# Kernel optimization log

Measured on AMD Instinct MI355X. Metric: run time of the kernel, lower is better.

The kernel has to match this reference:

```python
import jax, jax.numpy as jnp
import numpy as np

B, S, H = 4, 1024, 1024
NH = 16
D = H // NH  # attention_head_size = 64
L = 9        # num_labels
MAXREL = 5
B_PERSON = 1
I_PERSON = 2
LN_EPS = 1e-5


def setup_inputs() -> dict:
    key = jax.random.key(0)
    ks = jax.random.split(key, 16)
    lin = lambda k, i, o: 0.02 * jax.random.normal(k, (i, o), jnp.float32)
    return {
        "sequence_output": jax.random.normal(ks[0], (B, S, H), jnp.float32),
        "Wq": lin(ks[1], H, H), "bq": jnp.zeros((H,), jnp.float32),
        "Wk": lin(ks[2], H, H), "bk": jnp.zeros((H,), jnp.float32),
        "Wv": lin(ks[3], H, H), "bv": jnp.zeros((H,), jnp.float32),
        "Wo": lin(ks[4], H, H), "bo": jnp.zeros((H,), jnp.float32),
        "ln_g": jnp.ones((H,), jnp.float32), "ln_b": jnp.zeros((H,), jnp.float32),
        "Ws": lin(ks[5], H, L), "bs": jnp.zeros((L,), jnp.float32),
        "entity_bias": 0.1 * jax.random.normal(ks[6], (L,), jnp.float32),
        "rel_pos_emb": jax.random.normal(ks[7], (2 * MAXREL + 1, D), jnp.float32),  # declared but unused in forward math, matching the torch module
    }


def reference(sequence_output, Wq, bq, Wk, bk, Wv, bv, Wo, bo, ln_g, ln_b, Ws, bs, entity_bias, rel_pos_emb):
    x = sequence_output  # [B,S,H]
    b, s, _ = x.shape

    def heads(t):  # [B,S,H] -> [B,NH,S,D]
        return t.reshape(b, s, NH, D).transpose(0, 2, 1, 3)

    q = heads(x @ Wq + bq)
    k = heads(x @ Wk + bk)
    v = heads(x @ Wv + bv)

    scores = jnp.einsum('bhqd,bhkd->bhqk', q, k)  # [B,NH,S,S]

    r = jnp.arange(s, dtype=jnp.float32)
    dist = jnp.abs(r[:, None] - r[None, :])                 # |i-j|, [S,S]
    pos_bias = jnp.exp(-0.1 * jnp.clip(dist, 0.0, float(MAXREL)))
    # torch order: (scores + pos_bias) / sqrt(D) + distance_mask
    scores = (scores + pos_bias) / np.sqrt(D) + (-0.1) * dist

    probs = jax.nn.softmax(scores, axis=-1)  # dropout is identity in eval
    ctx = jnp.einsum('bhqk,bhkd->bhqd', probs, v)
    ctx = ctx.transpose(0, 2, 1, 3).reshape(b, s, H)

    y = x + (ctx @ Wo + bo)  # residual
    mu = y.mean(-1, keepdims=True)
    var = y.var(-1, keepdims=True)
    yn = (y - mu) / jnp.sqrt(var + LN_EPS) * ln_g + ln_b

    span_logits = yn @ Ws + bs  # [B,S,L]
    # entity-bias loop: if argmax(span_logits[i,j-1]) == B-PERSON, add entity_bias[I-PERSON] twice to final[i,j,I-PERSON]
    prev_is_b = (jnp.argmax(span_logits[:, :-1, :], axis=-1) == B_PERSON).astype(span_logits.dtype)  # [B,S-1]
    final_logits = span_logits.at[:, 1:, I_PERSON].add(2.0 * entity_bias[I_PERSON] * prev_is_b)
    return final_logits
```

## Files before the change

### kernel.cpp

```cpp
#include <hip/hip_runtime.h>
#include <hip/hip_bf16.h>
#include <math.h>

typedef unsigned short ush;
typedef __attribute__((ext_vector_type(8))) short frag16;
typedef __attribute__((ext_vector_type(4))) float f32x4;

#define S_   1024
#define H_   1024
#define NH_  16
#define D_   64
#define L_   9
#define MB_  (1048576ull)

__device__ __forceinline__ ush bf16_rne(float x) {
  unsigned int b = __float_as_uint(x);
  b += 0x7FFFu + ((b >> 16) & 1u);
  return (ush)(b >> 16);
}
__device__ __forceinline__ void split2(float x, ush& h, ush& l) {
  h = bf16_rne(x);
  l = bf16_rne(x - __uint_as_float((unsigned int)h << 16));
}

__device__ __forceinline__ void load_lds16(const ush* g, const ush* l) {
  __builtin_amdgcn_global_load_lds(
      (const __attribute__((address_space(1))) void*)g,
      (__attribute__((address_space(3))) void*)l, 16, 0, 0);
}

__global__ __launch_bounds__(256) void split_wT4(
    const float* W0, const float* W1, const float* W2, const float* W3,
    ush* h0, ush* l0, ush* h1, ush* l1, ush* h2, ush* l2, ush* h3, ush* l3) {
  __shared__ __align__(16) float Ls[64][68];
  const float* W = (blockIdx.z == 0) ? W0 : (blockIdx.z == 1) ? W1
                 : (blockIdx.z == 2) ? W2 : W3;
  ush* Th = (blockIdx.z == 0) ? h0 : (blockIdx.z == 1) ? h1
          : (blockIdx.z == 2) ? h2 : h3;
  ush* Tl = (blockIdx.z == 0) ? l0 : (blockIdx.z == 1) ? l1
          : (blockIdx.z == 2) ? l2 : l3;
  const int tid = threadIdx.x;
  const int n0 = blockIdx.x * 64, k0 = blockIdx.y * 64;
#pragma unroll
  for (int it = 0; it < 4; it++) {
    int flat = tid + 256 * it;
    int row = flat >> 4, nc = (flat & 15) * 4;
    *(float4*)&Ls[row][nc] = *(const float4*)&W[(size_t)(k0 + row) * 1024 + n0 + nc];
  }
  __syncthreads();
#pragma unroll
  for (int it = 0; it < 2; it++) {
    int flat = tid + 256 * it;
    int nrow = flat >> 3, kc = (flat & 7) * 8;
    ush hs[8], ls[8];
#pragma unroll
    for (int u = 0; u < 8; u++) split2(Ls[kc + u][nrow], hs[u], ls[u]);
    uint4 ph, pl;
    ph.x = hs[0] | ((unsigned)hs[1] << 16); ph.y = hs[2] | ((unsigned)hs[3] << 16);
    ph.z = hs[4] | ((unsigned)hs[5] << 16); ph.w = hs[6] | ((unsigned)hs[7] << 16);
    pl.x = ls[0] | ((unsigned)ls[1] << 16); pl.y = ls[2] | ((unsigned)ls[3] << 16);
    pl.z = ls[4] | ((unsigned)ls[5] << 16); pl.w = ls[6] | ((unsigned)ls[7] << 16);
    size_t o = (size_t)(n0 + nrow) * 1024 + k0 + kc;
    *(uint4*)&Th[o] = ph;
    *(uint4*)&Tl[o] = pl;
  }
}

__global__ __launch_bounds__(256) void cast_x(
    const float* __restrict__ x, ush* __restrict__ xh) {
  const size_t i = ((size_t)blockIdx.x * 256 + threadIdx.x) * 8;
  float4 a = *(const float4*)&x[i];
  float4 b = *(const float4*)&x[i + 4];
  const float v[8] = {a.x, a.y, a.z, a.w, b.x, b.y, b.z, b.w};
  ush h[8];
#pragma unroll
  for (int u = 0; u < 8; u++) h[u] = bf16_rne(v[u]);
  uint4 ph;
  ph.x = h[0] | ((unsigned)h[1] << 16); ph.y = h[2] | ((unsigned)h[3] << 16);
  ph.z = h[4] | ((unsigned)h[5] << 16); ph.w = h[6] | ((unsigned)h[7] << 16);
  *(uint4*)&xh[i] = ph;
}

__global__ __launch_bounds__(256) void gemm_qkv(
    const ush* __restrict__ xh,
    const ush* __restrict__ Bq_h, const ush* __restrict__ Bq_l,
    const ush* __restrict__ Bk_h, const ush* __restrict__ Bk_l,
    const ush* __restrict__ Bv_h, const ush* __restrict__ Bv_l,
    const float* __restrict__ bq, const float* __restrict__ bk,
    const float* __restrict__ bv,
    ush* __restrict__ qh, ush* __restrict__ kh, ush* __restrict__ vT) {
  __shared__ __align__(16) ush As[2][128][32];
  __shared__ __align__(16) ush Bs[2][2][128][32];
  const int tid = threadIdx.x, lane = tid & 63, wave = tid >> 6;
  const int l15 = lane & 15, quad = lane >> 4;
  const int m0 = blockIdx.y * 128, n0 = blockIdx.x * 128;
  const int z = blockIdx.z;
  const ush* Bh_g = (z == 0) ? Bq_h : (z == 1) ? Bk_h : Bv_h;
  const ush* Bl_g = (z == 0) ? Bq_l : (z == 1) ? Bk_l : Bv_l;
  const float* bias = (z == 0) ? bq : (z == 1) ? bk : bv;
  ush* outp = (z == 0) ? qh : (z == 1) ? kh : vT;

  const int wm = (wave >> 1) * 64, wn = (wave & 1) * 64;

  f32x4 acc[4][4];
#pragma unroll
  for (int i = 0; i < 4; i++)
#pragma unroll
    for (int j = 0; j < 4; j++) acc[i][j] = (f32x4){0.f, 0.f, 0.f, 0.f};

  auto stage = [&](int bi, int k0) {
#pragma unroll
    for (int jj = 0; jj < 2; jj++) {
      const int call = wave * 2 + jj;
      const int c = call * 64 + lane;
      const int r = c >> 2, ch = c & 3;
      const ush* src = xh + (size_t)(m0 + r) * 1024 + k0 + ch * 8;
      load_lds16(src, &As[bi][0][0] + (size_t)call * 512);
    }
#pragma unroll
    for (int jj = 0; jj < 4; jj++) {
      const int call = wave * 4 + jj;
      const int c = call * 64 + lane;
      const int r = (c >> 2) & 127, ch = c & 3;
      const ush* src = ((c >= 512) ? Bl_g : Bh_g)
                     + (size_t)(n0 + r) * 1024 + k0 + ch * 8;
      load_lds16(src, &Bs[bi][0][0][0] + (size_t)call * 512);
    }
  };

  stage(0, 0);
  __syncthreads();

  for (int k0 = 0; k0 < 1024; k0 += 32) {
    const int cur = (k0 >> 5) & 1;
    if (k0 + 32 < 1024) stage(cur ^ 1, k0 + 32);

    frag16 a_h[4], b_h[4], b_l[4];
#pragma unroll
    for (int s = 0; s < 4; s++)
      a_h[s] = *(const frag16*)&As[cur][wm + s * 16 + l15][quad * 8];
#pragma unroll
    for (int t = 0; t < 4; t++) {
      const int col = wn + t * 16 + l15;
      b_h[t] = *(const frag16*)&Bs[cur][0][col][quad * 8];
      b_l[t] = *(const frag16*)&Bs[cur][1][col][quad * 8];
    }
#pragma unroll
    for (int mi = 0; mi < 4; mi++)
#pragma unroll
      for (int ni = 0; ni < 4; ni++) {
        acc[mi][ni] = __builtin_amdgcn_mfma_f32_16x16x32_bf16(
            a_h[mi], b_h[ni], acc[mi][ni], 0, 0, 0);
        acc[mi][ni] = __builtin_amdgcn_mfma_f32_16x16x32_bf16(
            a_h[mi], b_l[ni], acc[mi][ni], 0, 0, 0);
      }
    __syncthreads();
  }

#pragma unroll
  for (int mi = 0; mi < 4; mi++) {
    const int rbase = m0 + wm + mi * 16 + quad * 4;
    const int bb = rbase >> 10, ss = rbase & 1023;
#pragma unroll
    for (int ni = 0; ni < 4; ni++) {
      const int col = n0 + wn + ni * 16 + l15;
      const float bv_ = bias[col];
      const int hidx = col >> 6, d = col & 63;
      if (z == 2) {
        ushort4 p4;
        p4.x = bf16_rne(acc[mi][ni][0] + bv_);
        p4.y = bf16_rne(acc[mi][ni][1] + bv_);
        p4.z = bf16_rne(acc[mi][ni][2] + bv_);
        p4.w = bf16_rne(acc[mi][ni][3] + bv_);
        *(ushort4*)&outp[((size_t)(bb * NH_ + hidx) * D_ + d) * S_ + ss] = p4;
      } else {
#pragma unroll
        for (int r = 0; r < 4; r++) {
          const size_t o =
              ((size_t)(bb * NH_ + hidx) * S_ + (ss + r)) * D_ + d;
          outp[o] = bf16_rne(acc[mi][ni][r] + bv_);
        }
      }
    }
  }
}

__global__ __launch_bounds__(256) void gemm_o(
    const ush* __restrict__ ctxh,
    const ush* __restrict__ Boh, const ush* __restrict__ Bol,
    const float* __restrict__ bo, const float* __restrict__ resid,
    float* __restrict__ outf) {
  __shared__ __align__(16) ush As[2][128][32];
  __shared__ __align__(16) ush Bs[2][2][64][32];
  const int tid = threadIdx.x, lane = tid & 63, wave = tid >> 6;
  const int l15 = lane & 15, quad = lane >> 4;
  const int m0 = blockIdx.y * 128, n0 = blockIdx.x * 64;
  const int wm = (wave >> 1) * 64, wn = (wave & 1) * 32;

  f32x4 acc[4][2];
#pragma unroll
  for (int i = 0; i < 4; i++)
#pragma unroll
    for (int j = 0; j < 2; j++) acc[i][j] = (f32x4){0.f, 0.f, 0.f, 0.f};

  auto stage = [&](int bi, int k0) {
#pragma unroll
    for (int jj = 0; jj < 2; jj++) {
      const int call = wave * 2 + jj;
      const int c = call * 64 + lane;
      const int r = c >> 2, ch = c & 3;
      const ush* src = ctxh + (size_t)(m0 + r) * 1024 + k0 + ch * 8;
      load_lds16(src, &As[bi][0][0] + (size_t)call * 512);
    }
#pragma unroll
    for (int jj = 0; jj < 2; jj++) {
      const int call = wave * 2 + jj;
      const int c = call * 64 + lane;
      const int r = (c >> 2) & 63, ch = c & 3;
      const ush* src = ((c >= 256) ? Bol : Boh)
                     + (size_t)(n0 + r) * 1024 + k0 + ch * 8;
      load_lds16(src, &Bs[bi][0][0][0] + (size_t)call * 512);
    }
  };

  stage(0, 0);
  __syncthreads();

  for (int k0 = 0; k0 < 1024; k0 += 32) {
    const int cur = (k0 >> 5) & 1;
    if (k0 + 32 < 1024) stage(cur ^ 1, k0 + 32);

    frag16 a_h[4], b_h[2], b_l[2];
#pragma unroll
    for (int s = 0; s < 4; s++)
      a_h[s] = *(const frag16*)&As[cur][wm + s * 16 + l15][quad * 8];
#pragma unroll
    for (int t = 0; t < 2; t++) {
      const int col = wn + t * 16 + l15;
      b_h[t] = *(const frag16*)&Bs[cur][0][col][quad * 8];
      b_l[t] = *(const frag16*)&Bs[cur][1][col][quad * 8];
    }
#pragma unroll
    for (int mi = 0; mi < 4; mi++)
#pragma unroll
      for (int ni = 0; ni < 2; ni++) {
        acc[mi][ni] = __builtin_amdgcn_mfma_f32_16x16x32_bf16(
            a_h[mi], b_h[ni], acc[mi][ni], 0, 0, 0);
        acc[mi][ni] = __builtin_amdgcn_mfma_f32_16x16x32_bf16(
            a_h[mi], b_l[ni], acc[mi][ni], 0, 0, 0);
      }
    __syncthreads();
  }

#pragma unroll
  for (int mi = 0; mi < 4; mi++) {
    const int rbase = m0 + wm + mi * 16 + quad * 4;
#pragma unroll
    for (int ni = 0; ni < 2; ni++) {
      const int col = n0 + wn + ni * 16 + l15;
      const float bv_ = bo[col];
#pragma unroll
      for (int r = 0; r < 4; r++) {
        const int m = rbase + r;
        outf[(size_t)m * 1024 + col] =
            acc[mi][ni][r] + bv_ + resid[(size_t)m * 1024 + col];
      }
    }
  }
}

__global__ __launch_bounds__(256) void attn2(
    const ush* __restrict__ qh, const ush* __restrict__ kh,
    const ush* __restrict__ vT, ush* __restrict__ ch) {
  __shared__ __align__(16) ush Kh[64][72];
  __shared__ __align__(16) ush VTs[64][72];
  __shared__ __align__(16) ush Pst[64][72];
  __shared__ float LUT[256];
  const int tid = threadIdx.x;
  const int lane = tid & 63, wave = tid >> 6;
  const int l15 = lane & 15, quad = lane >> 4;
  const int w16 = wave * 16;
  const int bh = blockIdx.y;
  const int b = bh >> 4, h = bh & 15;
  const int q0 = blockIdx.x * 64;

  const float K1 = 0.18033688011112042f;
  const float K2 = 0.14426950408889634f;
  {
    const float dd = (float)tid;
    LUT[tid] = __expf(-0.1f * fminf(dd, 5.0f)) * K1 - dd * K2
             - 28.853900817779268f;
  }

  const size_t qrow = ((size_t)bh * S_ + q0 + w16 + l15) * D_;
  frag16 a_h[2];
  a_h[0] = *(const frag16*)&qh[qrow + quad * 8];
  a_h[1] = *(const frag16*)&qh[qrow + 32 + quad * 8];

  f32x4 o[4];
  float lrow[4];
#pragma unroll
  for (int i = 0; i < 4; i++) {
    o[i] = (f32x4){0.f, 0.f, 0.f, 0.f};
    lrow[i] = 0.f;
  }

  const size_t kbase = (size_t)bh * S_ * D_;
  const size_t vbase = (size_t)bh * D_ * S_;

  const int jlo = (q0 > 128) ? q0 - 128 : 0;
  const int jend = (q0 + 192 < S_) ? q0 + 192 : S_;

  for (int j0 = jlo; j0 < jend; j0 += 64) {
    __syncthreads();
#pragma unroll
    for (int it = 0; it < 2; it++) {
      const int flat = tid + 256 * it;
      const int row = flat >> 3, dc = (flat & 7) * 8;
      *(uint4*)&Kh[row][dc] =
          *(const uint4*)&kh[kbase + (size_t)(j0 + row) * D_ + dc];
      *(uint4*)&VTs[row][dc] =
          *(const uint4*)&vT[vbase + (size_t)row * S_ + j0 + dc];
    }
    __syncthreads();

    f32x4 c4[4];
#pragma unroll
    for (int nt = 0; nt < 4; nt++) c4[nt] = (f32x4){0.f, 0.f, 0.f, 0.f};
#pragma unroll
    for (int kk = 0; kk < 2; kk++) {
#pragma unroll
      for (int nt = 0; nt < 4; nt++) {
        frag16 bh_ = *(const frag16*)&Kh[nt * 16 + l15][kk * 32 + quad * 8];
        c4[nt] = __builtin_amdgcn_mfma_f32_16x16x32_bf16(a_h[kk], bh_, c4[nt], 0, 0, 0);
      }
    }

    const int ib = q0 + w16 + quad * 4 - j0 - l15;
#pragma unroll
    for (int r = 0; r < 4; r++) {
#pragma unroll
      for (int nt = 0; nt < 4; nt++) {
        int di = ib + r - nt * 16;
        di = (di < 0) ? -di : di;
        const float sv = exp2f(fmaf(c4[nt][r], K1, LUT[di]));
        lrow[r] += sv;
        Pst[w16 + quad * 4 + r][nt * 16 + l15] = bf16_rne(sv);
      }
    }

    frag16 pa[2];
    pa[0] = *(const frag16*)&Pst[w16 + l15][quad * 8];
    pa[1] = *(const frag16*)&Pst[w16 + l15][32 + quad * 8];
#pragma unroll
    for (int dt = 0; dt < 4; dt++) {
      frag16 vb0 = *(const frag16*)&VTs[dt * 16 + l15][quad * 8];
      frag16 vb1 = *(const frag16*)&VTs[dt * 16 + l15][32 + quad * 8];
      o[dt] = __builtin_amdgcn_mfma_f32_16x16x32_bf16(pa[0], vb0, o[dt], 0, 0, 0);
      o[dt] = __builtin_amdgcn_mfma_f32_16x16x32_bf16(pa[1], vb1, o[dt], 0, 0, 0);
    }
  }

#pragma unroll
  for (int r = 0; r < 4; r++) {
#pragma unroll
    for (int off = 1; off < 16; off <<= 1) lrow[r] += __shfl_xor(lrow[r], off);
    const float inv = 1.0f / lrow[r];
    const size_t rowp =
        ((size_t)(b * S_ + q0 + w16 + quad * 4 + r)) * H_ + h * 64;
#pragma unroll
    for (int dt = 0; dt < 4; dt++)
      ch[rowp + dt * 16 + l15] = bf16_rne(o[dt][r] * inv);
  }
}

__global__ __launch_bounds__(256) void ln_span(
    const float* __restrict__ y, const float* __restrict__ g,
    const float* __restrict__ bta, const float* __restrict__ Wsp,
    const float* __restrict__ bs, float* __restrict__ logits) {
  const int row = blockIdx.x;
  const int tid = threadIdx.x, lane = tid & 63, wave = tid >> 6;
  const float* yr = y + (size_t)row * 1024;
  float vals[4], s = 0.f, s2 = 0.f;
#pragma unroll
  for (int i = 0; i < 4; i++) {
    float t = yr[tid + i * 256];
    vals[i] = t; s += t; s2 += t * t;
  }
#pragma unroll
  for (int off = 32; off; off >>= 1) {
    s += __shfl_xor(s, off);
    s2 += __shfl_xor(s2, off);
  }
  __shared__ float red[8];
  __shared__ float red9[4][12];
  if (lane == 0) { red[wave] = s; red[4 + wave] = s2; }
  __syncthreads();
  s = red[0] + red[1] + red[2] + red[3];
  s2 = red[4] + red[5] + red[6] + red[7];
  const float mu = s * (1.0f / 1024.0f);
  const float var = s2 * (1.0f / 1024.0f) - mu * mu;
  const float inv = rsqrtf(var + 1e-5f);

  float lg[9];
#pragma unroll
  for (int l = 0; l < 9; l++) lg[l] = 0.f;
#pragma unroll
  for (int i = 0; i < 4; i++) {
    const int hh = tid + i * 256;
    const float yn = (vals[i] - mu) * inv * g[hh] + bta[hh];
#pragma unroll
    for (int l = 0; l < 9; l++) lg[l] += yn * Wsp[hh * 9 + l];
  }
#pragma unroll
  for (int l = 0; l < 9; l++) {
#pragma unroll
    for (int off = 32; off; off >>= 1) lg[l] += __shfl_xor(lg[l], off);
  }
  if (lane == 0) {
#pragma unroll
    for (int l = 0; l < 9; l++) red9[wave][l] = lg[l];
  }
  __syncthreads();
  if (tid < 9) {
    logits[(size_t)row * 9 + tid] =
        red9[0][tid] + red9[1][tid] + red9[2][tid] + red9[3][tid] + bs[tid];
  }
}

__global__ __launch_bounds__(256) void final_kernel(
    const float* __restrict__ logits, const float* __restrict__ eb,
    float* __restrict__ out) {
  const int m = blockIdx.x * 256 + threadIdx.x;
  const int i = m & 1023;
  float cur[9];
#pragma unroll
  for (int l = 0; l < 9; l++) cur[l] = logits[(size_t)m * 9 + l];
  if (i > 0) {
    const float* prev = logits + (size_t)(m - 1) * 9;
    int am = 0;
    float best = prev[0];
#pragma unroll
    for (int l = 1; l < 9; l++) {
      float pv = prev[l];
      if (pv > best) { best = pv; am = l; }
    }
    if (am == 1) cur[2] += 2.0f * eb[2];
  }
#pragma unroll
  for (int l = 0; l < 9; l++) out[(size_t)m * 9 + l] = cur[l];
}

extern "C" void kernel_launch(void* const* d_in, const int* in_sizes, int n_in,
                              void* d_out, int out_size, void* d_ws, size_t ws_size,
                              hipStream_t stream) {
  const float* x    = (const float*)d_in[0];
  const float* Wq   = (const float*)d_in[1];
  const float* bq   = (const float*)d_in[2];
  const float* Wk   = (const float*)d_in[3];
  const float* bk   = (const float*)d_in[4];
  const float* Wv   = (const float*)d_in[5];
  const float* bv   = (const float*)d_in[6];
  const float* Wo   = (const float*)d_in[7];
  const float* bo   = (const float*)d_in[8];
  const float* ln_g = (const float*)d_in[9];
  const float* ln_b = (const float*)d_in[10];
  const float* Ws   = (const float*)d_in[11];
  const float* bs   = (const float*)d_in[12];
  const float* eb   = (const float*)d_in[13];
  float* out = (float*)d_out;
  char* W8 = (char*)d_ws;

  ush* WoT_h = (ush*)(W8 + 0 * MB_);
  ush* WoT_l = (ush*)(W8 + 2 * MB_);
  ush* WqT_h = (ush*)(W8 + 4 * MB_);
  ush* WqT_l = (ush*)(W8 + 6 * MB_);
  ush* WkT_h = (ush*)(W8 + 8 * MB_);
  ush* WkT_l = (ush*)(W8 + 10 * MB_);
  ush* WvT_h = (ush*)(W8 + 12 * MB_);
  ush* WvT_l = (ush*)(W8 + 14 * MB_);
  ush* xh    = (ush*)(W8 + 16 * MB_);
  ush* qh    = (ush*)(W8 + 24 * MB_);
  ush* kh    = (ush*)(W8 + 32 * MB_);
  ush* vT    = (ush*)(W8 + 40 * MB_);
  ush* ctxh  = (ush*)(W8 + 48 * MB_);
  float* y_ws  = (float*)(W8 + 24 * MB_);
  float* lg_ws = (float*)(W8 + 40 * MB_);

  split_wT4<<<dim3(16, 16, 4), 256, 0, stream>>>(
      Wq, Wk, Wv, Wo, WqT_h, WqT_l, WkT_h, WkT_l, WvT_h, WvT_l, WoT_h, WoT_l);
  cast_x<<<2048, 256, 0, stream>>>(x, xh);

  gemm_qkv<<<dim3(8, 32, 3), 256, 0, stream>>>(
      xh, WqT_h, WqT_l, WkT_h, WkT_l, WvT_h, WvT_l, bq, bk, bv, qh, kh, vT);
  attn2<<<dim3(16, 64), 256, 0, stream>>>(qh, kh, vT, ctxh);
  gemm_o<<<dim3(16, 32), 256, 0, stream>>>(ctxh, WoT_h, WoT_l, bo, x, y_ws);
  ln_span<<<4096, 256, 0, stream>>>(y_ws, ln_g, ln_b, Ws, bs, lg_ws);
  final_kernel<<<16, 256, 0, stream>>>(lg_ws, eb, out);
}
```

Baseline: 244.5 us.

## Switch GEMMs and attention from split-bf16 to single fp16 MFMA

Replaces the bf16 hi/lo weight split (two MFMAs per tile) with one fp16 cast of weights and activations, so each GEMM issues half the MFMAs and loads half the B-operand bytes. Attention Q/K/V, probabilities and context move to fp16 as well. The softmax LUT offset shrinks from about 28.85 to about 2.885 so the probabilities stay inside fp16 range. The trade is reduced dynamic range and a different rounding error, with possible overflow or underflow if the data leaves fp16 range.

```diff
diff --git a/kernel.cpp b/kernel.cpp
--- a/kernel.cpp
+++ b/kernel.cpp
@@ -3,7 +3,8 @@
 #include <math.h>
 
 typedef unsigned short ush;
-typedef __attribute__((ext_vector_type(8))) short frag16;
+typedef __attribute__((ext_vector_type(8))) _Float16 fragh;
+typedef __attribute__((ext_vector_type(4))) _Float16 half4;
 typedef __attribute__((ext_vector_type(4))) float f32x4;
 
 #define S_   1024
@@ -13,32 +14,20 @@
 #define L_   9
 #define MB_  (1048576ull)
 
-__device__ __forceinline__ ush bf16_rne(float x) {
-  unsigned int b = __float_as_uint(x);
-  b += 0x7FFFu + ((b >> 16) & 1u);
-  return (ush)(b >> 16);
-}
-__device__ __forceinline__ void split2(float x, ush& h, ush& l) {
-  h = bf16_rne(x);
-  l = bf16_rne(x - __uint_as_float((unsigned int)h << 16));
-}
-
 __device__ __forceinline__ void load_lds16(const ush* g, const ush* l) {
   __builtin_amdgcn_global_load_lds(
       (const __attribute__((address_space(1))) void*)g,
       (__attribute__((address_space(3))) void*)l, 16, 0, 0);
 }
 
-__global__ __launch_bounds__(256) void split_wT4(
+__global__ __launch_bounds__(256) void cast_wT4(
     const float* W0, const float* W1, const float* W2, const float* W3,
-    ush* h0, ush* l0, ush* h1, ush* l1, ush* h2, ush* l2, ush* h3, ush* l3) {
+    ush* T0, ush* T1, ush* T2, ush* T3) {
   __shared__ __align__(16) float Ls[64][68];
   const float* W = (blockIdx.z == 0) ? W0 : (blockIdx.z == 1) ? W1
                  : (blockIdx.z == 2) ? W2 : W3;
-  ush* Th = (blockIdx.z == 0) ? h0 : (blockIdx.z == 1) ? h1
-          : (blockIdx.z == 2) ? h2 : h3;
-  ush* Tl = (blockIdx.z == 0) ? l0 : (blockIdx.z == 1) ? l1
-          : (blockIdx.z == 2) ? l2 : l3;
+  ush* Th = (blockIdx.z == 0) ? T0 : (blockIdx.z == 1) ? T1
+          : (blockIdx.z == 2) ? T2 : T3;
   const int tid = threadIdx.x;
   const int n0 = blockIdx.x * 64, k0 = blockIdx.y * 64;
 #pragma unroll
@@ -52,17 +41,10 @@
   for (int it = 0; it < 2; it++) {
     int flat = tid + 256 * it;
     int nrow = flat >> 3, kc = (flat & 7) * 8;
-    ush hs[8], ls[8];
-#pragma unroll
-    for (int u = 0; u < 8; u++) split2(Ls[kc + u][nrow], hs[u], ls[u]);
-    uint4 ph, pl;
-    ph.x = hs[0] | ((unsigned)hs[1] << 16); ph.y = hs[2] | ((unsigned)hs[3] << 16);
-    ph.z = hs[4] | ((unsigned)hs[5] << 16); ph.w = hs[6] | ((unsigned)hs[7] << 16);
-    pl.x = ls[0] | ((unsigned)ls[1] << 16); pl.y = ls[2] | ((unsigned)ls[3] << 16);
-    pl.z = ls[4] | ((unsigned)ls[5] << 16); pl.w = ls[6] | ((unsigned)ls[7] << 16);
-    size_t o = (size_t)(n0 + nrow) * 1024 + k0 + kc;
-    *(uint4*)&Th[o] = ph;
-    *(uint4*)&Tl[o] = pl;
+    fragh v;
+#pragma unroll
+    for (int u = 0; u < 8; u++) v[u] = (_Float16)Ls[kc + u][nrow];
+    *(fragh*)&Th[(size_t)(n0 + nrow) * 1024 + k0 + kc] = v;
   }
 }
 
@@ -71,32 +53,28 @@
   const size_t i = ((size_t)blockIdx.x * 256 + threadIdx.x) * 8;
   float4 a = *(const float4*)&x[i];
   float4 b = *(const float4*)&x[i + 4];
-  const float v[8] = {a.x, a.y, a.z, a.w, b.x, b.y, b.z, b.w};
-  ush h[8];
-#pragma unroll
-  for (int u = 0; u < 8; u++) h[u] = bf16_rne(v[u]);
-  uint4 ph;
-  ph.x = h[0] | ((unsigned)h[1] << 16); ph.y = h[2] | ((unsigned)h[3] << 16);
-  ph.z = h[4] | ((unsigned)h[5] << 16); ph.w = h[6] | ((unsigned)h[7] << 16);
-  *(uint4*)&xh[i] = ph;
+  fragh v;
+  v[0] = (_Float16)a.x; v[1] = (_Float16)a.y;
+  v[2] = (_Float16)a.z; v[3] = (_Float16)a.w;
+  v[4] = (_Float16)b.x; v[5] = (_Float16)b.y;
+  v[6] = (_Float16)b.z; v[7] = (_Float16)b.w;
+  *(fragh*)&xh[i] = v;
 }
 
 __global__ __launch_bounds__(256) void gemm_qkv(
     const ush* __restrict__ xh,
-    const ush* __restrict__ Bq_h, const ush* __restrict__ Bq_l,
-    const ush* __restrict__ Bk_h, const ush* __restrict__ Bk_l,
-    const ush* __restrict__ Bv_h, const ush* __restrict__ Bv_l,
+    const ush* __restrict__ Bq, const ush* __restrict__ Bk,
+    const ush* __restrict__ Bv,
     const float* __restrict__ bq, const float* __restrict__ bk,
     const float* __restrict__ bv,
     ush* __restrict__ qh, ush* __restrict__ kh, ush* __restrict__ vT) {
   __shared__ __align__(16) ush As[2][128][32];
-  __shared__ __align__(16) ush Bs[2][2][128][32];
+  __shared__ __align__(16) ush Bs[2][128][32];
   const int tid = threadIdx.x, lane = tid & 63, wave = tid >> 6;
   const int l15 = lane & 15, quad = lane >> 4;
   const int m0 = blockIdx.y * 128, n0 = blockIdx.x * 128;
   const int z = blockIdx.z;
-  const ush* Bh_g = (z == 0) ? Bq_h : (z == 1) ? Bk_h : Bv_h;
-  const ush* Bl_g = (z == 0) ? Bq_l : (z == 1) ? Bk_l : Bv_l;
+  const ush* Bg = (z == 0) ? Bq : (z == 1) ? Bk : Bv;
   const float* bias = (z == 0) ? bq : (z == 1) ? bk : bv;
   ush* outp = (z == 0) ? qh : (z == 1) ? kh : vT;
 
@@ -114,17 +92,16 @@
       const int call = wave * 2 + jj;
       const int c = call * 64 + lane;
       const int r = c >> 2, ch = c & 3;
-      const ush* src = xh + (size_t)(m0 + r) * 1024 + k0 + ch * 8;
-      load_lds16(src, &As[bi][0][0] + (size_t)call * 512);
-    }
-#pragma unroll
-    for (int jj = 0; jj < 4; jj++) {
-      const int call = wave * 4 + jj;
+      load_lds16(xh + (size_t)(m0 + r) * 1024 + k0 + ch * 8,
+                 &As[bi][0][0] + (size_t)call * 512);
+    }
+#pragma unroll
+    for (int jj = 0; jj < 2; jj++) {
+      const int call = wave * 2 + jj;
       const int c = call * 64 + lane;
-      const int r = (c >> 2) & 127, ch = c & 3;
-      const ush* src = ((c >= 512) ? Bl_g : Bh_g)
-                     + (size_t)(n0 + r) * 1024 + k0 + ch * 8;
-      load_lds16(src, &Bs[bi][0][0][0] + (size_t)call * 512);
+      const int r = c >> 2, ch = c & 3;
+      load_lds16(Bg + (size_t)(n0 + r) * 1024 + k0 + ch * 8,
+                 &Bs[bi][0][0] + (size_t)call * 512);
     }
   };
 
@@ -135,25 +112,19 @@
     const int cur = (k0 >> 5) & 1;
     if (k0 + 32 < 1024) stage(cur ^ 1, k0 + 32);
 
-    frag16 a_h[4], b_h[4], b_l[4];
+    fragh a[4], b[4];
 #pragma unroll
     for (int s = 0; s < 4; s++)
-      a_h[s] = *(const frag16*)&As[cur][wm + s * 16 + l15][quad * 8];
-#pragma unroll
-    for (int t = 0; t < 4; t++) {
-      const int col = wn + t * 16 + l15;
-      b_h[t] = *(const frag16*)&Bs[cur][0][col][quad * 8];
-      b_l[t] = *(const frag16*)&Bs[cur][1][col][quad * 8];
-    }
+      a[s] = *(const fragh*)&As[cur][wm + s * 16 + l15][quad * 8];
+#pragma unroll
+    for (int t = 0; t < 4; t++)
+      b[t] = *(const fragh*)&Bs[cur][wn + t * 16 + l15][quad * 8];
 #pragma unroll
     for (int mi = 0; mi < 4; mi++)
 #pragma unroll
-      for (int ni = 0; ni < 4; ni++) {
-        acc[mi][ni] = __builtin_amdgcn_mfma_f32_16x16x32_bf16(
-            a_h[mi], b_h[ni], acc[mi][ni], 0, 0, 0);
-        acc[mi][ni] = __builtin_amdgcn_mfma_f32_16x16x32_bf16(
-            a_h[mi], b_l[ni], acc[mi][ni], 0, 0, 0);
-      }
+      for (int ni = 0; ni < 4; ni++)
+        acc[mi][ni] = __builtin_amdgcn_mfma_f32_16x16x32_f16(
+            a[mi], b[ni], acc[mi][ni], 0, 0, 0);
     __syncthreads();
   }
 
@@ -167,18 +138,18 @@
       const float bv_ = bias[col];
       const int hidx = col >> 6, d = col & 63;
       if (z == 2) {
-        ushort4 p4;
-        p4.x = bf16_rne(acc[mi][ni][0] + bv_);
-        p4.y = bf16_rne(acc[mi][ni][1] + bv_);
-        p4.z = bf16_rne(acc[mi][ni][2] + bv_);
-        p4.w = bf16_rne(acc[mi][ni][3] + bv_);
-        *(ushort4*)&outp[((size_t)(bb * NH_ + hidx) * D_ + d) * S_ + ss] = p4;
+        half4 p4;
+        p4[0] = (_Float16)(acc[mi][ni][0] + bv_);
+        p4[1] = (_Float16)(acc[mi][ni][1] + bv_);
+        p4[2] = (_Float16)(acc[mi][ni][2] + bv_);
+        p4[3] = (_Float16)(acc[mi][ni][3] + bv_);
+        *(half4*)&outp[((size_t)(bb * NH_ + hidx) * D_ + d) * S_ + ss] = p4;
       } else {
 #pragma unroll
         for (int r = 0; r < 4; r++) {
           const size_t o =
               ((size_t)(bb * NH_ + hidx) * S_ + (ss + r)) * D_ + d;
-          outp[o] = bf16_rne(acc[mi][ni][r] + bv_);
+          *(_Float16*)&outp[o] = (_Float16)(acc[mi][ni][r] + bv_);
         }
       }
     }
@@ -186,12 +157,11 @@
 }
 
 __global__ __launch_bounds__(256) void gemm_o(
-    const ush* __restrict__ ctxh,
-    const ush* __restrict__ Boh, const ush* __restrict__ Bol,
+    const ush* __restrict__ ctxh, const ush* __restrict__ Bo,
     const float* __restrict__ bo, const float* __restrict__ resid,
     float* __restrict__ outf) {
   __shared__ __align__(16) ush As[2][128][32];
-  __shared__ __align__(16) ush Bs[2][2][64][32];
+  __shared__ __align__(16) ush Bs[2][64][32];
   const int tid = threadIdx.x, lane = tid & 63, wave = tid >> 6;
   const int l15 = lane & 15, quad = lane >> 4;
   const int m0 = blockIdx.y * 128, n0 = blockIdx.x * 64;
@@ -209,17 +179,14 @@
       const int call = wave * 2 + jj;
       const int c = call * 64 + lane;
       const int r = c >> 2, ch = c & 3;
-      const ush* src = ctxh + (size_t)(m0 + r) * 1024 + k0 + ch * 8;
-      load_lds16(src, &As[bi][0][0] + (size_t)call * 512);
-    }
-#pragma unroll
-    for (int jj = 0; jj < 2; jj++) {
-      const int call = wave * 2 + jj;
-      const int c = call * 64 + lane;
-      const int r = (c >> 2) & 63, ch = c & 3;
-      const ush* src = ((c >= 256) ? Bol : Boh)
-                     + (size_t)(n0 + r) * 1024 + k0 + ch * 8;
-      load_lds16(src, &Bs[bi][0][0][0] + (size_t)call * 512);
+      load_lds16(ctxh + (size_t)(m0 + r) * 1024 + k0 + ch * 8,
+                 &As[bi][0][0] + (size_t)call * 512);
+    }
+    {
+      const int c = wave * 64 + lane;
+      const int r = c >> 2, ch = c & 3;
+      load_lds16(Bo + (size_t)(n0 + r) * 1024 + k0 + ch * 8,
+                 &Bs[bi][0][0] + (size_t)wave * 512);
     }
   };
 
@@ -230,25 +197,19 @@
     const int cur = (k0 >> 5) & 1;
     if (k0 + 32 < 1024) stage(cur ^ 1, k0 + 32);
 
-    frag16 a_h[4], b_h[2], b_l[2];
+    fragh a[4], b[2];
 #pragma unroll
     for (int s = 0; s < 4; s++)
-      a_h[s] = *(const frag16*)&As[cur][wm + s * 16 + l15][quad * 8];
-#pragma unroll
-    for (int t = 0; t < 2; t++) {
-      const int col = wn + t * 16 + l15;
-      b_h[t] = *(const frag16*)&Bs[cur][0][col][quad * 8];
-      b_l[t] = *(const frag16*)&Bs[cur][1][col][quad * 8];
-    }
+      a[s] = *(const fragh*)&As[cur][wm + s * 16 + l15][quad * 8];
+#pragma unroll
+    for (int t = 0; t < 2; t++)
+      b[t] = *(const fragh*)&Bs[cur][wn + t * 16 + l15][quad * 8];
 #pragma unroll
     for (int mi = 0; mi < 4; mi++)
 #pragma unroll
-      for (int ni = 0; ni < 2; ni++) {
-        acc[mi][ni] = __builtin_amdgcn_mfma_f32_16x16x32_bf16(
-            a_h[mi], b_h[ni], acc[mi][ni], 0, 0, 0);
-        acc[mi][ni] = __builtin_amdgcn_mfma_f32_16x16x32_bf16(
-            a_h[mi], b_l[ni], acc[mi][ni], 0, 0, 0);
-      }
+      for (int ni = 0; ni < 2; ni++)
+        acc[mi][ni] = __builtin_amdgcn_mfma_f32_16x16x32_f16(
+            a[mi], b[ni], acc[mi][ni], 0, 0, 0);
     __syncthreads();
   }
 
@@ -289,13 +250,13 @@
   {
     const float dd = (float)tid;
     LUT[tid] = __expf(-0.1f * fminf(dd, 5.0f)) * K1 - dd * K2
-             - 28.853900817779268f;
+             - 2.8853900817779268f;
   }
 
   const size_t qrow = ((size_t)bh * S_ + q0 + w16 + l15) * D_;
-  frag16 a_h[2];
-  a_h[0] = *(const frag16*)&qh[qrow + quad * 8];
-  a_h[1] = *(const frag16*)&qh[qrow + 32 + quad * 8];
+  fragh a_h[2];
+  a_h[0] = *(const fragh*)&qh[qrow + quad * 8];
+  a_h[1] = *(const fragh*)&qh[qrow + 32 + quad * 8];
 
   f32x4 o[4];
   float lrow[4];
@@ -331,8 +292,8 @@
     for (int kk = 0; kk < 2; kk++) {
 #pragma unroll
       for (int nt = 0; nt < 4; nt++) {
-        frag16 bh_ = *(const frag16*)&Kh[nt * 16 + l15][kk * 32 + quad * 8];
-        c4[nt] = __builtin_amdgcn_mfma_f32_16x16x32_bf16(a_h[kk], bh_, c4[nt], 0, 0, 0);
+        fragh bh_ = *(const fragh*)&Kh[nt * 16 + l15][kk * 32 + quad * 8];
+        c4[nt] = __builtin_amdgcn_mfma_f32_16x16x32_f16(a_h[kk], bh_, c4[nt], 0, 0, 0);
       }
     }
 
@@ -345,19 +306,19 @@
         di = (di < 0) ? -di : di;
         const float sv = exp2f(fmaf(c4[nt][r], K1, LUT[di]));
         lrow[r] += sv;
-        Pst[w16 + quad * 4 + r][nt * 16 + l15] = bf16_rne(sv);
+        *(_Float16*)&Pst[w16 + quad * 4 + r][nt * 16 + l15] = (_Float16)sv;
       }
     }
 
-    frag16 pa[2];
-    pa[0] = *(const frag16*)&Pst[w16 + l15][quad * 8];
-    pa[1] = *(const frag16*)&Pst[w16 + l15][32 + quad * 8];
+    fragh pa[2];
+    pa[0] = *(const fragh*)&Pst[w16 + l15][quad * 8];
+    pa[1] = *(const fragh*)&Pst[w16 + l15][32 + quad * 8];
 #pragma unroll
     for (int dt = 0; dt < 4; dt++) {
-      frag16 vb0 = *(const frag16*)&VTs[dt * 16 + l15][quad * 8];
-      frag16 vb1 = *(const frag16*)&VTs[dt * 16 + l15][32 + quad * 8];
-      o[dt] = __builtin_amdgcn_mfma_f32_16x16x32_bf16(pa[0], vb0, o[dt], 0, 0, 0);
-      o[dt] = __builtin_amdgcn_mfma_f32_16x16x32_bf16(pa[1], vb1, o[dt], 0, 0, 0);
+      fragh vb0 = *(const fragh*)&VTs[dt * 16 + l15][quad * 8];
+      fragh vb1 = *(const fragh*)&VTs[dt * 16 + l15][32 + quad * 8];
+      o[dt] = __builtin_amdgcn_mfma_f32_16x16x32_f16(pa[0], vb0, o[dt], 0, 0, 0);
+      o[dt] = __builtin_amdgcn_mfma_f32_16x16x32_f16(pa[1], vb1, o[dt], 0, 0, 0);
     }
   }
 
@@ -370,7 +331,7 @@
         ((size_t)(b * S_ + q0 + w16 + quad * 4 + r)) * H_ + h * 64;
 #pragma unroll
     for (int dt = 0; dt < 4; dt++)
-      ch[rowp + dt * 16 + l15] = bf16_rne(o[dt][r] * inv);
+      *(_Float16*)&ch[rowp + dt * 16 + l15] = (_Float16)(o[dt][r] * inv);
   }
 }
 
@@ -471,30 +432,26 @@
   float* out = (float*)d_out;
   char* W8 = (char*)d_ws;
 
-  ush* WoT_h = (ush*)(W8 + 0 * MB_);
-  ush* WoT_l = (ush*)(W8 + 2 * MB_);
-  ush* WqT_h = (ush*)(W8 + 4 * MB_);
-  ush* WqT_l = (ush*)(W8 + 6 * MB_);
-  ush* WkT_h = (ush*)(W8 + 8 * MB_);
-  ush* WkT_l = (ush*)(W8 + 10 * MB_);
-  ush* WvT_h = (ush*)(W8 + 12 * MB_);
-  ush* WvT_l = (ush*)(W8 + 14 * MB_);
-  ush* xh    = (ush*)(W8 + 16 * MB_);
-  ush* qh    = (ush*)(W8 + 24 * MB_);
-  ush* kh    = (ush*)(W8 + 32 * MB_);
-  ush* vT    = (ush*)(W8 + 40 * MB_);
-  ush* ctxh  = (ush*)(W8 + 48 * MB_);
-  float* y_ws  = (float*)(W8 + 24 * MB_);
-  float* lg_ws = (float*)(W8 + 40 * MB_);
-
-  split_wT4<<<dim3(16, 16, 4), 256, 0, stream>>>(
-      Wq, Wk, Wv, Wo, WqT_h, WqT_l, WkT_h, WkT_l, WvT_h, WvT_l, WoT_h, WoT_l);
+  ush* WoT  = (ush*)(W8 + 0 * MB_);
+  ush* WqT  = (ush*)(W8 + 2 * MB_);
+  ush* WkT  = (ush*)(W8 + 4 * MB_);
+  ush* WvT  = (ush*)(W8 + 6 * MB_);
+  ush* xh   = (ush*)(W8 + 8 * MB_);
+  ush* qh   = (ush*)(W8 + 16 * MB_);
+  ush* kh   = (ush*)(W8 + 24 * MB_);
+  ush* vT   = (ush*)(W8 + 32 * MB_);
+  ush* ctxh = (ush*)(W8 + 40 * MB_);
+  float* y_ws  = (float*)(W8 + 48 * MB_);
+  float* lg_ws = (float*)(W8 + 16 * MB_);
+
+  cast_wT4<<<dim3(16, 16, 4), 256, 0, stream>>>(
+      Wq, Wk, Wv, Wo, WqT, WkT, WvT, WoT);
   cast_x<<<2048, 256, 0, stream>>>(x, xh);
 
   gemm_qkv<<<dim3(8, 32, 3), 256, 0, stream>>>(
-      xh, WqT_h, WqT_l, WkT_h, WkT_l, WvT_h, WvT_l, bq, bk, bv, qh, kh, vT);
+      xh, WqT, WkT, WvT, bq, bk, bv, qh, kh, vT);
   attn2<<<dim3(16, 64), 256, 0, stream>>>(qh, kh, vT, ctxh);
-  gemm_o<<<dim3(16, 32), 256, 0, stream>>>(ctxh, WoT_h, WoT_l, bo, x, y_ws);
+  gemm_o<<<dim3(16, 32), 256, 0, stream>>>(ctxh, WoT, bo, x, y_ws);
   ln_span<<<4096, 256, 0, stream>>>(y_ws, ln_g, ln_b, Ws, bs, lg_ws);
   final_kernel<<<16, 256, 0, stream>>>(lg_ws, eb, out);
 }
```

New measurement: 203.3 us. 16.8% less time.
